# Optimization experiments

Measured on AMD Instinct MI355X. Metric: run time of the kernel, lower is better.

The kernel has to match this reference:

```python
import jax, jax.numpy as jnp
import numpy as np

ENZ_DIM, CPD_DIM, OUT_DIM = 1280, 256, 512
B, L_ENZ, L_CPD = 32, 512, 128
SCALE = OUT_DIM ** 0.5


def _linear_params(key, d_in, d_out):
    k1, k2 = jax.random.split(key)
    lim = 1.0 / np.sqrt(d_in)
    W = jax.random.uniform(k1, (d_in, d_out), jnp.float32, -lim, lim)
    b = jax.random.uniform(k2, (d_out,), jnp.float32, -lim, lim)
    return W, b


def setup_inputs() -> dict:
    key = jax.random.key(0)
    ks = jax.random.split(key, 16)
    inp = {
        "enz_node_feature": jax.random.normal(ks[0], (B, L_ENZ, ENZ_DIM), jnp.float32),
        "substrate_node_feature": jax.random.normal(ks[1], (B, L_CPD, CPD_DIM), jnp.float32),
        "product_node_feature": jax.random.normal(ks[2], (B, L_CPD, CPD_DIM), jnp.float32),
        "enz_node_feature_mask": jnp.ones((B, L_ENZ), dtype=bool),
        "substrate_node_feature_mask": jnp.ones((B, L_CPD), dtype=bool),
        "product_node_feature_mask": jnp.ones((B, L_CPD), dtype=bool),
        "interaction_weight": jax.random.normal(ks[3], (B, L_CPD, L_ENZ), jnp.float32),
    }
    # cross_attn_enzyme: query=enz (ENZ_DIM), key/value=cpd (CPD_DIM)
    inp["enz_Wq"], inp["enz_bq"] = _linear_params(ks[4], ENZ_DIM, OUT_DIM)
    inp["enz_Wk"], inp["enz_bk"] = _linear_params(ks[5], CPD_DIM, OUT_DIM)
    inp["enz_Wv"], inp["enz_bv"] = _linear_params(ks[6], CPD_DIM, OUT_DIM)
    # cross_attn_substrate: query=cpd, key/value=enz
    inp["sub_Wq"], inp["sub_bq"] = _linear_params(ks[7], CPD_DIM, OUT_DIM)
    inp["sub_Wk"], inp["sub_bk"] = _linear_params(ks[8], ENZ_DIM, OUT_DIM)
    inp["sub_Wv"], inp["sub_bv"] = _linear_params(ks[9], ENZ_DIM, OUT_DIM)
    # cross_attn_product: query=cpd, key/value=enz
    inp["prod_Wq"], inp["prod_bq"] = _linear_params(ks[10], CPD_DIM, OUT_DIM)
    inp["prod_Wk"], inp["prod_bk"] = _linear_params(ks[11], ENZ_DIM, OUT_DIM)
    inp["prod_Wv"], inp["prod_bv"] = _linear_params(ks[12], ENZ_DIM, OUT_DIM)
    return inp


def _cross_attn(q_in, k_in, v_in, q_mask, k_mask, Wq, bq, Wk, bk, Wv, bv, attn_bias=None):
    q = q_in @ Wq + bq          # [B, Lq, D]
    k = k_in @ Wk + bk          # [B, Lk, D]
    v = v_in @ Wv + bv          # [B, Lk, D]
    scores = jnp.einsum("bqd,bkd->bqk", q, k) / SCALE
    if attn_bias is not None:
        scores = scores + attn_bias
    mask = q_mask[:, :, None] & k_mask[:, None, :]   # [B, Lq, Lk]
    scores = jnp.where(mask, scores, -1e9)
    w = jax.nn.softmax(scores, axis=-1)
    return jnp.einsum("bqk,bkd->bqd", w, v)


def reference(enz_node_feature, substrate_node_feature, product_node_feature,
              enz_node_feature_mask, substrate_node_feature_mask, product_node_feature_mask,
              interaction_weight,
              enz_Wq, enz_bq, enz_Wk, enz_bk, enz_Wv, enz_bv,
              sub_Wq, sub_bq, sub_Wk, sub_bk, sub_Wv, sub_bv,
              prod_Wq, prod_bq, prod_Wk, prod_bk, prod_Wv, prod_bv):
    subs_pocket_weight = interaction_weight                       # [B, L_cpd, L_enz]
    pocket_subs_weight = jnp.swapaxes(interaction_weight, 1, 2)   # [B, L_enz, L_cpd]

    enzyme_subs = _cross_attn(enz_node_feature, substrate_node_feature, substrate_node_feature,
                              enz_node_feature_mask, substrate_node_feature_mask,
                              enz_Wq, enz_bq, enz_Wk, enz_bk, enz_Wv, enz_bv,
                              attn_bias=pocket_subs_weight)
    subs_enzyme = _cross_attn(substrate_node_feature, enz_node_feature, enz_node_feature,
                              substrate_node_feature_mask, enz_node_feature_mask,
                              sub_Wq, sub_bq, sub_Wk, sub_bk, sub_Wv, sub_bv,
                              attn_bias=subs_pocket_weight)
    # product path reuses cross_attn_enzyme weights for enz->prod (as in torch code)
    enzyme_prod = _cross_attn(enz_node_feature, product_node_feature, product_node_feature,
                              enz_node_feature_mask, product_node_feature_mask,
                              enz_Wq, enz_bq, enz_Wk, enz_bk, enz_Wv, enz_bv)
    prod_enzyme = _cross_attn(product_node_feature, enz_node_feature, enz_node_feature,
                              product_node_feature_mask, enz_node_feature_mask,
                              prod_Wq, prod_bq, prod_Wk, prod_bk, prod_Wv, prod_bv)

    return jnp.concatenate([enzyme_subs.mean(axis=1), subs_enzyme.mean(axis=1),
                            enzyme_prod.mean(axis=1), prod_enzyme.mean(axis=1)], axis=-1)
```

## Files before the change

kernel.cpp:

```cpp
#include <hip/hip_runtime.h>
#include <cstdint>
#include <cstddef>


#define SCALE_INV 0.044194173824159216f

typedef short bf16x8 __attribute__((ext_vector_type(8)));
typedef float f32x4  __attribute__((ext_vector_type(4)));

__device__ __forceinline__ ushort f2bf(float f) {
  union { float f; unsigned u; } c; c.f = f;
  unsigned u = c.u + 0x7fffu + ((c.u >> 16) & 1u);
  return (ushort)(u >> 16);
}
__device__ __forceinline__ float bf2f(ushort h) {
  return __uint_as_float(((unsigned)h) << 16);
}
__device__ __forceinline__ void gload16(const ushort* g, ushort* l) {
  __builtin_amdgcn_global_load_lds(
      (const __attribute__((address_space(1))) void*)g,
      (__attribute__((address_space(3))) void*)l, 16, 0, 0);
}

__device__ __forceinline__ void cvt8(const float* __restrict__ in,
                                     ushort* __restrict__ out, int blk, int n) {
  int i = (blk * 256 + (int)threadIdx.x) * 8;
  if (i >= n) return;
  float4 a = *(const float4*)(in + i);
  float4 b = *(const float4*)(in + i + 4);
  ushort o[8] = { f2bf(a.x), f2bf(a.y), f2bf(a.z), f2bf(a.w),
                  f2bf(b.x), f2bf(b.y), f2bf(b.z), f2bf(b.w) };
  *(uint4*)(out + i) = *(uint4*)o;
}

__global__ __launch_bounds__(256) void prep_fused(
    const float* __restrict__ enz, const float* __restrict__ sub,
    const float* __restrict__ prod,
    ushort* __restrict__ enz_b, ushort* __restrict__ sub_b, ushort* __restrict__ prod_b,
    const float* __restrict__ enz_Wq, const float* __restrict__ enz_Wk,
    const float* __restrict__ sub_Wq, const float* __restrict__ sub_Wk,
    const float* __restrict__ prod_Wq, const float* __restrict__ prod_Wk,
    ushort* __restrict__ eWq_b, ushort* __restrict__ eWk_b,
    ushort* __restrict__ sWq_b, ushort* __restrict__ sWk_b,
    ushort* __restrict__ pWq_b, ushort* __restrict__ pWk_b,
    const float* __restrict__ enz_bq, const float* __restrict__ sub_bq,
    const float* __restrict__ prod_bq,
    const float* __restrict__ enz_bv, const float* __restrict__ sub_bv,
    const float* __restrict__ prod_bv,
    ushort* __restrict__ W3t, float* __restrict__ u_e_s,
    float* __restrict__ zero_base, float* __restrict__ out)
{
  const int f = blockIdx.x, t = threadIdx.x;
  if (f < 10240) { cvt8(enz, enz_b, f, 20971520); return; }
  if (f < 10752) { cvt8(sub, sub_b, f - 10240, 1048576); return; }
  if (f < 11264) { cvt8(prod, prod_b, f - 10752, 1048576); return; }
  if (f < 12416) {
    const int l = f - 11264;
    if (l < 320)       cvt8(enz_Wq,  eWq_b, l,        655360);
    else if (l < 640)  cvt8(sub_Wk,  sWk_b, l - 320,  655360);
    else if (l < 960)  cvt8(prod_Wk, pWk_b, l - 640,  655360);
    else if (l < 1024) cvt8(enz_Wk,  eWk_b, l - 960,  131072);
    else if (l < 1088) cvt8(sub_Wq,  sWq_b, l - 1024, 131072);
    else               cvt8(prod_Wq, pWq_b, l - 1088, 131072);
    return;
  }
  if (f < 12592) {
    const int g = f - 12416;
    const float* W; const float* bv; int d0, kind;
    if (g < 80)       { W = sub_Wk;  bv = sub_bq;  d0 = g * 16;         kind = 0; }
    else if (g < 160) { W = prod_Wk; bv = prod_bq; d0 = (g - 80) * 16;  kind = 1; }
    else              { W = enz_Wk;  bv = enz_bq;  d0 = (g - 160) * 16; kind = 2; }
    const int r = t >> 4, i = t & 15, d = d0 + r;
    const float* row = W + (size_t)d * 512;
    float s = 0.f;
#pragma unroll
    for (int j = 0; j < 32; j++) s += row[i + j * 16] * bv[i + j * 16];
    s += __shfl_xor(s, 1); s += __shfl_xor(s, 2);
    s += __shfl_xor(s, 4); s += __shfl_xor(s, 8);
    if (i == 0) {
      if (kind < 2) W3t[(size_t)(768 + kind) * 1280 + d] = f2bf(s);
      else          u_e_s[d] = s * SCALE_INV;
    }
    return;
  }
  if (f < 13168) { zero_base[(f - 12592) * 256 + t] = 0.f; return; }
  if (f < 13483) {
    const int idx = (f - 13168) * 256 + t;
    ((unsigned*)(W3t + (size_t)770 * 1280))[idx] = 0u;
    return;
  }
  {
    const int idx = (f - 13483) * 256 + t;
    const int col = idx & 2047;
    const int q = col >> 9, n = col & 511;
    const float* bvp = (q == 1) ? sub_bv : (q == 3) ? prod_bv : enz_bv;
    out[idx] = bvp[n];
  }
}

__device__ __forceinline__ void mfma_tile(
    const ushort* __restrict__ A, int lda,
    const ushort* __restrict__ Bt, int ldb, int K,
    int bm, int bn, ushort* AsBase, ushort* BsBase, f32x4 (&acc)[4][4])
{
  const int t = threadIdx.x, wave = t >> 6, lane = t & 63;
  const int srow = wave * 16 + (lane >> 2);
  const int sseg = (lane & 3) * 8;
  const ushort* Ag0 = A + (size_t)(bm + srow) * lda + sseg;
  const ushort* Ag1 = Ag0 + (size_t)64 * lda;
  const ushort* Bg0 = Bt + (size_t)(bn + srow) * ldb + sseg;
  const ushort* Bg1 = Bg0 + (size_t)64 * ldb;
  ushort* AsP0 = AsBase + srow * 32 + sseg;
  ushort* AsP1 = AsP0 + 64 * 32;
  ushort* BsP0 = BsBase + srow * 32 + sseg;
  ushort* BsP1 = BsP0 + 64 * 32;
  const int wm = (wave >> 1) * 64, wn = (wave & 1) * 64;
  const int fl = lane & 15, fq = lane >> 4;
  const bf16x8* ArP = (const bf16x8*)(AsBase + (wm + fl) * 32 + fq * 8);
  const bf16x8* BrP = (const bf16x8*)(BsBase + (wn + fl) * 32 + fq * 8);
  for (int k0 = 0; k0 < K; k0 += 32) {
    __syncthreads();
    gload16(Ag0 + k0, AsP0);
    gload16(Ag1 + k0, AsP1);
    gload16(Bg0 + k0, BsP0);
    gload16(Bg1 + k0, BsP1);
    __syncthreads();
    bf16x8 af[4], bfr[4];
#pragma unroll
    for (int i = 0; i < 4; i++) af[i] = ArP[i * 64];
#pragma unroll
    for (int j = 0; j < 4; j++) bfr[j] = BrP[j * 64];
#pragma unroll
    for (int i = 0; i < 4; i++)
#pragma unroll
      for (int j = 0; j < 4; j++)
        acc[i][j] = __builtin_amdgcn_mfma_f32_16x16x32_bf16(af[i], bfr[j], acc[i][j], 0, 0, 0);
  }
}

__global__ __launch_bounds__(256) void fold_w3(
    const ushort* __restrict__ eWq_b, const ushort* __restrict__ eWk_b,
    const ushort* __restrict__ sWq_b, const ushort* __restrict__ sWk_b,
    const ushort* __restrict__ pWq_b, const ushort* __restrict__ pWk_b,
    ushort* __restrict__ W3t)
{
  __shared__ __align__(16) ushort As[128 * 32];
  __shared__ __align__(16) ushort Bs[128 * 32];
  const int f = blockIdx.x, seg = f / 20, l = f % 20;
  const int bm = (l / 10) * 128, bn = (l % 10) * 128;
  const ushort* A  = (seg == 0) ? eWk_b : (seg == 1) ? sWq_b : pWq_b;
  const ushort* Bt = (seg == 0) ? eWq_b : (seg == 1) ? sWk_b : pWk_b;
  f32x4 acc[4][4] = {};
  mfma_tile(A, 512, Bt, 512, 512, bm, bn, As, Bs, acc);
  const int lane = threadIdx.x & 63, wave = threadIdx.x >> 6;
  const int wm = (wave >> 1) * 64, wn = (wave & 1) * 64;
  const int fl = lane & 15, fq = lane >> 4;
#pragma unroll
  for (int i = 0; i < 4; i++)
#pragma unroll
    for (int j = 0; j < 4; j++) {
      const int col = bn + wn + j * 16 + fl;
#pragma unroll
      for (int r = 0; r < 4; r++) {
        const int row = seg * 256 + bm + wm + i * 16 + fq * 4 + r;
        W3t[(size_t)row * 1280 + col] = f2bf(acc[i][j][r]);
      }
    }
}

__global__ __launch_bounds__(256) void y_gemm(
    const ushort* __restrict__ enz_b, const ushort* __restrict__ W3t,
    ushort* __restrict__ Y)
{
  __shared__ __align__(16) ushort As[128 * 32];
  __shared__ __align__(16) ushort Bs[128 * 32];
  const int f = blockIdx.x;
  const int xcd = f & 7, slot = f >> 3;
  const int bm = (xcd * 16 + slot / 7) * 128, bn = (slot % 7) * 128;
  f32x4 acc[4][4] = {};
  mfma_tile(enz_b, 1280, W3t, 1280, 1280, bm, bn, As, Bs, acc);
  const int lane = threadIdx.x & 63, wave = threadIdx.x >> 6;
  const int wm = (wave >> 1) * 64, wn = (wave & 1) * 64;
  const int fl = lane & 15, fq = lane >> 4;
#pragma unroll
  for (int i = 0; i < 4; i++)
#pragma unroll
    for (int j = 0; j < 4; j++) {
      const int col = bn + wn + j * 16 + fl;
#pragma unroll
      for (int r = 0; r < 4; r++) {
        const int row = bm + wm + i * 16 + fq * 4 + r;
        Y[(size_t)row * 896 + col] = f2bf(acc[i][j][r]);
      }
    }
}

__global__ __launch_bounds__(256) void score_fused(
    const ushort* __restrict__ Y, const ushort* __restrict__ sub_b,
    const ushort* __restrict__ prod_b, const float* __restrict__ iw,
    const float* __restrict__ u_e_s,
    float* __restrict__ Sc_se, float* __restrict__ Sc_pe,
    float* __restrict__ l_se, float* __restrict__ l_pe,
    float* __restrict__ wsum_es, float* __restrict__ wsum_ep)
{
  __shared__ __align__(16) ushort As[128 * 32];
  __shared__ __align__(16) ushort Bs[128 * 32];
  __shared__ float red[2][128];
  __shared__ float red2[2][128];
  __shared__ float tsh[128];
  const int f = blockIdx.x, t = threadIdx.x;
  const int lane = t & 63, wave = t >> 6;
  const int wm = (wave >> 1) * 64, wn = (wave & 1) * 64;
  const int fl = lane & 15, fq = lane >> 4;
  f32x4 acc[4][4] = {};

  if (f < 256) {
    const int path = f >> 7, l = f & 127, b = l & 31, mt = l >> 5;
    const int bm = mt * 128;
    const ushort* X = (path ? prod_b : sub_b) + (size_t)b * 32768;
    {
      const int col = t >> 1, half = t & 1;
      const ushort* xr = X + col * 256 + half * 128;
      const float* uu = u_e_s + half * 128;
      float s = 0.f;
      for (int c = 0; c < 128; c++) s += bf2f(xr[c]) * uu[c];
      s += __shfl_xor(s, 1);
      if (!half) tsh[col] = s;
    }
    mfma_tile(Y + (size_t)b * 512 * 896, 896, X, 256, 256, bm, 0, As, Bs, acc);
    const size_t ib = (size_t)b * 65536;
    float rsum[4][4];
#pragma unroll
    for (int i = 0; i < 4; i++)
#pragma unroll
      for (int r = 0; r < 4; r++) rsum[i][r] = 0.f;
#pragma unroll
    for (int i = 0; i < 4; i++)
#pragma unroll
      for (int j = 0; j < 4; j++)
#pragma unroll
        for (int r = 0; r < 4; r++) {
          const int row = wm + i * 16 + fq * 4 + r;
          const int col = wn + j * 16 + fl;
          float s = acc[i][j][r] * SCALE_INV + tsh[col];
          if (path == 0) s += iw[ib + (size_t)col * 512 + (bm + row)];
          const float e = __expf(s);
          acc[i][j][r] = e;
          rsum[i][r] += e;
        }
#pragma unroll
    for (int m = 1; m <= 8; m <<= 1)
#pragma unroll
      for (int i = 0; i < 4; i++)
#pragma unroll
        for (int r = 0; r < 4; r++)
          rsum[i][r] += __shfl_xor(rsum[i][r], m);
    if (fl == 0)
#pragma unroll
      for (int i = 0; i < 4; i++)
#pragma unroll
        for (int r = 0; r < 4; r++)
          red[wave & 1][wm + i * 16 + fq * 4 + r] = rsum[i][r];
    __syncthreads();
    float csum[4] = { 0.f, 0.f, 0.f, 0.f };
#pragma unroll
    for (int i = 0; i < 4; i++)
#pragma unroll
      for (int r = 0; r < 4; r++) {
        const int row = wm + i * 16 + fq * 4 + r;
        const float invr = 1.f / (red[0][row] + red[1][row]);
#pragma unroll
        for (int j = 0; j < 4; j++) csum[j] += acc[i][j][r] * invr;
      }
#pragma unroll
    for (int m = 16; m <= 32; m <<= 1)
#pragma unroll
      for (int j = 0; j < 4; j++) csum[j] += __shfl_xor(csum[j], m);
    if (fq == 0)
#pragma unroll
      for (int j = 0; j < 4; j++) red2[wave >> 1][wn + j * 16 + fl] = csum[j];
    __syncthreads();
    float* ws = (path ? wsum_ep : wsum_es) + b * 128;
    if (t < 128) atomicAdd(&ws[t], red2[0][t] + red2[1][t]);
  } else {
    const int g = f - 256, path = g >> 7, l = g & 127, b = l & 31, nt = l >> 5;
    const int bn = nt * 128;
    const ushort* A  = (path ? prod_b : sub_b) + (size_t)b * 32768;
    const ushort* Bt = Y + (size_t)b * 512 * 896 + 256 + path * 256;
    mfma_tile(A, 256, Bt, 896, 256, 0, bn, As, Bs, acc);
    const size_t ib = (size_t)b * 65536;
    float* Sc = (path ? Sc_pe : Sc_se) + ib;
    float tv[4];
#pragma unroll
    for (int j = 0; j < 4; j++) {
      const int col = wn + j * 16 + fl;
      tv[j] = bf2f(Y[(size_t)(b * 512 + bn + col) * 896 + 768 + path]) * SCALE_INV;
    }
    float rsum[4][4];
#pragma unroll
    for (int i = 0; i < 4; i++)
#pragma unroll
      for (int r = 0; r < 4; r++) rsum[i][r] = 0.f;
#pragma unroll
    for (int i = 0; i < 4; i++)
#pragma unroll
      for (int j = 0; j < 4; j++)
#pragma unroll
        for (int r = 0; r < 4; r++) {
          const int row = wm + i * 16 + fq * 4 + r;
          const int col = wn + j * 16 + fl;
          float s = acc[i][j][r] * SCALE_INV + tv[j];
          if (path == 0) s += iw[ib + (size_t)row * 512 + (bn + col)];
          const float e = __expf(s);
          Sc[(size_t)row * 512 + bn + col] = e;
          rsum[i][r] += e;
        }
#pragma unroll
    for (int m = 1; m <= 8; m <<= 1)
#pragma unroll
      for (int i = 0; i < 4; i++)
#pragma unroll
        for (int r = 0; r < 4; r++)
          rsum[i][r] += __shfl_xor(rsum[i][r], m);
    if (fl == 0)
#pragma unroll
      for (int i = 0; i < 4; i++)
#pragma unroll
        for (int r = 0; r < 4; r++)
          red[wave & 1][wm + i * 16 + fq * 4 + r] = rsum[i][r];
    __syncthreads();
    float* lr = (path ? l_pe : l_se) + b * 128;
    if (t < 128) atomicAdd(&lr[t], red[0][t] + red[1][t]);
  }
}

__global__ __launch_bounds__(256) void colsum2(
    const float* __restrict__ Sc_se, const float* __restrict__ Sc_pe,
    const float* __restrict__ l_se, const float* __restrict__ l_pe,
    float* __restrict__ wsum_se, float* __restrict__ wsum_pe)
{
  __shared__ float inv[32];
  const int f = blockIdx.x, t = threadIdx.x;
  const int path = f >> 7, l = f & 127, b = l & 31, qc = l >> 5;
  const float* Sc = (path ? Sc_pe : Sc_se) + (size_t)b * 65536 + (size_t)(qc * 32) * 512;
  const float* lv = (path ? l_pe : l_se) + b * 128 + qc * 32;
  float* ws = (path ? wsum_pe : wsum_se) + b * 512;
  if (t < 32) inv[t] = 1.f / lv[t];
  __syncthreads();
  float a0 = 0.f, a1 = 0.f;
  for (int q = 0; q < 32; q++) {
    const float iq = inv[q];
    a0 += Sc[(size_t)q * 512 + t] * iq;
    a1 += Sc[(size_t)q * 512 + 256 + t] * iq;
  }
  atomicAdd(&ws[t], a0);
  atomicAdd(&ws[t + 256], a1);
}

__global__ __launch_bounds__(256) void wx_fused(
    const float* __restrict__ wsum_se, const float* __restrict__ wsum_pe,
    const float* __restrict__ wsum_es, const float* __restrict__ wsum_ep,
    const ushort* __restrict__ enz_b, const ushort* __restrict__ sub_b,
    const ushort* __restrict__ prod_b,
    float* __restrict__ wx_se, float* __restrict__ wx_pe,
    float* __restrict__ wx_es, float* __restrict__ wx_ep)
{
  __shared__ float wse[256], wpe[256];
  const int f = blockIdx.x, t = threadIdx.x;
  if (f < 320) {
    const int ch = f % 5, tmp = f / 5, b = tmp & 31, kh = tmp >> 5;
    wse[t] = wsum_se[b * 512 + kh * 256 + t];
    wpe[t] = wsum_pe[b * 512 + kh * 256 + t];
    __syncthreads();
    const int c = ch * 256 + t;
    const ushort* X = enz_b + (size_t)b * 512 * 1280 + (size_t)(kh * 256) * 1280 + c;
    float a_se = 0.f, a_pe = 0.f;
    for (int k = 0; k < 256; k++) {
      const float x = bf2f(X[(size_t)k * 1280]);
      a_se += wse[k] * x;
      a_pe += wpe[k] * x;
    }
    atomicAdd(&wx_se[b * 1280 + c], a_se);
    atomicAdd(&wx_pe[b * 1280 + c], a_pe);
  } else if (f < 352) {
    const int b = f - 320;
    const ushort* X = sub_b + (size_t)b * 128 * 256 + t;
    float a = 0.f;
    for (int k = 0; k < 128; k++) a += wsum_es[b * 128 + k] * bf2f(X[(size_t)k * 256]);
    wx_es[b * 256 + t] = a;
  } else {
    const int b = f - 352;
    const ushort* X = prod_b + (size_t)b * 128 * 256 + t;
    float a = 0.f;
    for (int k = 0; k < 128; k++) a += wsum_ep[b * 128 + k] * bf2f(X[(size_t)k * 256]);
    wx_ep[b * 256 + t] = a;
  }
}

__global__ __launch_bounds__(256) void out_gemv(
    const float* __restrict__ wx_es, const float* __restrict__ wx_se,
    const float* __restrict__ wx_ep, const float* __restrict__ wx_pe,
    const float* __restrict__ enz_Wv, const float* __restrict__ sub_Wv,
    const float* __restrict__ prod_Wv,
    float* __restrict__ out)
{
  __shared__ float sw[32][64];
  const int f = blockIdx.x, t = threadIdx.x;
  const float* wx; const float* Wv; int Cdim, qoff, nb, cc; float inv;
  if (f < 40)      { wx = wx_se; Wv = sub_Wv;  Cdim = 1280; inv = 1.f / 128.f; qoff = 512;  nb = f & 1;        cc = f >> 1; }
  else if (f < 80) { wx = wx_pe; Wv = prod_Wv; Cdim = 1280; inv = 1.f / 128.f; qoff = 1536; nb = (f - 40) & 1; cc = (f - 40) >> 1; }
  else if (f < 88) { wx = wx_es; Wv = enz_Wv;  Cdim = 256;  inv = 1.f / 512.f; qoff = 0;    nb = (f - 80) & 1; cc = (f - 80) >> 1; }
  else             { wx = wx_ep; Wv = enz_Wv;  Cdim = 256;  inv = 1.f / 512.f; qoff = 1024; nb = (f - 88) & 1; cc = (f - 88) >> 1; }
  const int c0 = cc * 64, n = nb * 256 + t;
#pragma unroll
  for (int i = 0; i < 8; i++) {
    const int idx = t + i * 256, b = idx >> 6, c = idx & 63;
    sw[b][c] = wx[(size_t)b * Cdim + c0 + c];
  }
  __syncthreads();
  float acc[32];
#pragma unroll
  for (int b = 0; b < 32; b++) acc[b] = 0.f;
  for (int c = 0; c < 64; c += 4) {
    const float w0 = Wv[(size_t)(c0 + c) * 512 + n];
    const float w1 = Wv[(size_t)(c0 + c + 1) * 512 + n];
    const float w2 = Wv[(size_t)(c0 + c + 2) * 512 + n];
    const float w3 = Wv[(size_t)(c0 + c + 3) * 512 + n];
#pragma unroll
    for (int b = 0; b < 32; b++) {
      const float4 s = *(const float4*)&sw[b][c];
      acc[b] += s.x * w0 + s.y * w1 + s.z * w2 + s.w * w3;
    }
  }
#pragma unroll
  for (int b = 0; b < 32; b++)
    atomicAdd(&out[(size_t)b * 2048 + qoff + n], acc[b] * inv);
}

extern "C" void kernel_launch(void* const* d_in, const int* in_sizes, int n_in,
                              void* d_out, int out_size, void* d_ws, size_t ws_size,
                              hipStream_t stream)
{
  (void)in_sizes; (void)n_in; (void)out_size; (void)ws_size;
  const float* enz     = (const float*)d_in[0];
  const float* sub     = (const float*)d_in[1];
  const float* prod    = (const float*)d_in[2];
  const float* iw      = (const float*)d_in[6];
  const float* enz_Wq  = (const float*)d_in[7];
  const float* enz_bq  = (const float*)d_in[8];
  const float* enz_Wk  = (const float*)d_in[9];
  const float* enz_Wv  = (const float*)d_in[11];
  const float* enz_bv  = (const float*)d_in[12];
  const float* sub_Wq  = (const float*)d_in[13];
  const float* sub_bq  = (const float*)d_in[14];
  const float* sub_Wk  = (const float*)d_in[15];
  const float* sub_Wv  = (const float*)d_in[17];
  const float* sub_bv  = (const float*)d_in[18];
  const float* prod_Wq = (const float*)d_in[19];
  const float* prod_bq = (const float*)d_in[20];
  const float* prod_Wk = (const float*)d_in[21];
  const float* prod_Wv = (const float*)d_in[23];
  const float* prod_bv = (const float*)d_in[24];
  float* out = (float*)d_out;

  char* wsb = (char*)d_ws;
  size_t off = 0;
  auto alloc = [&](size_t bytes) {
    void* p = wsb + off;
    off += (bytes + 255) & ~(size_t)255;
    return p;
  };
  ushort* enz_b   = (ushort*)alloc((size_t)32 * 512 * 1280 * 2);
  ushort* sub_b   = (ushort*)alloc((size_t)32 * 128 * 256 * 2);
  ushort* prod_b  = (ushort*)alloc((size_t)32 * 128 * 256 * 2);
  ushort* eWq_b   = (ushort*)alloc((size_t)1280 * 512 * 2);
  ushort* sWk_b   = (ushort*)alloc((size_t)1280 * 512 * 2);
  ushort* pWk_b   = (ushort*)alloc((size_t)1280 * 512 * 2);
  ushort* eWk_b   = (ushort*)alloc((size_t)256 * 512 * 2);
  ushort* sWq_b   = (ushort*)alloc((size_t)256 * 512 * 2);
  ushort* pWq_b   = (ushort*)alloc((size_t)256 * 512 * 2);
  ushort* W3t     = (ushort*)alloc((size_t)896 * 1280 * 2);
  ushort* Y       = (ushort*)alloc((size_t)16384 * 896 * 2);
  float*  u_e_s   = (float*)alloc(256 * 4);
  float*  Sc_se   = (float*)alloc((size_t)32 * 128 * 512 * 4);
  float*  Sc_pe   = (float*)alloc((size_t)32 * 128 * 512 * 4);
  float* wsum_es = (float*)alloc(4096 * 4);
  float* wsum_ep = (float*)alloc(4096 * 4);
  float* wsum_se = (float*)alloc(16384 * 4);
  float* wsum_pe = (float*)alloc(16384 * 4);
  float* l_se    = (float*)alloc(4096 * 4);
  float* l_pe    = (float*)alloc(4096 * 4);
  float* wx_se   = (float*)alloc(40960 * 4);
  float* wx_pe   = (float*)alloc(40960 * 4);
  float* wx_es   = (float*)alloc(8192 * 4);
  float* wx_ep   = (float*)alloc(8192 * 4);

  const dim3 blk(256);

  prep_fused<<<13739, blk, 0, stream>>>(
      enz, sub, prod, enz_b, sub_b, prod_b,
      enz_Wq, enz_Wk, sub_Wq, sub_Wk, prod_Wq, prod_Wk,
      eWq_b, eWk_b, sWq_b, sWk_b, pWq_b, pWk_b,
      enz_bq, sub_bq, prod_bq, enz_bv, sub_bv, prod_bv,
      W3t, u_e_s, wsum_es, out);

  fold_w3<<<60, blk, 0, stream>>>(eWq_b, eWk_b, sWq_b, sWk_b, pWq_b, pWk_b, W3t);

  y_gemm<<<896, blk, 0, stream>>>(enz_b, W3t, Y);

  score_fused<<<512, blk, 0, stream>>>(
      Y, sub_b, prod_b, iw, u_e_s, Sc_se, Sc_pe, l_se, l_pe, wsum_es, wsum_ep);

  colsum2<<<256, blk, 0, stream>>>(Sc_se, Sc_pe, l_se, l_pe, wsum_se, wsum_pe);

  wx_fused<<<384, blk, 0, stream>>>(
      wsum_se, wsum_pe, wsum_es, wsum_ep, enz_b, sub_b, prod_b,
      wx_se, wx_pe, wx_es, wx_ep);

  out_gemv<<<96, blk, 0, stream>>>(
      wx_es, wx_se, wx_ep, wx_pe, enz_Wv, sub_Wv, prod_Wv, out);
}
```

Baseline: 333.3 us.

## Rewrite y_gemm as 256x256 tile, 512-thread, double-buffered async-LDS GEMM

Replaces the 128x128 y_gemm built on the shared mfma_tile helper with a dedicated 256x256-tile kernel. It uses 8 waves, 128KB of dynamic LDS with double buffering, XOR-swizzled LDS layout, direct global-to-LDS loads and wave priority hints. The Y and W3t row pitch is padded from 896 to 1024 so N tiles divide evenly, and waves with nothing to do in the final partial tile skip their MFMAs. Downstream kernels and the zero-fill range are updated for the new pitch. This raises arithmetic intensity and overlaps loads with compute, at the cost of larger padded buffers, extra zeroing, and wasted tiles in the last N block.

```diff
diff --git a/kernel.cpp b/kernel.cpp
--- a/kernel.cpp
+++ b/kernel.cpp
@@ -84,13 +84,13 @@
     return;
   }
   if (f < 13168) { zero_base[(f - 12592) * 256 + t] = 0.f; return; }
-  if (f < 13483) {
+  if (f < 13803) {
     const int idx = (f - 13168) * 256 + t;
     ((unsigned*)(W3t + (size_t)770 * 1280))[idx] = 0u;
     return;
   }
   {
-    const int idx = (f - 13483) * 256 + t;
+    const int idx = (f - 13803) * 256 + t;
     const int col = idx & 2047;
     const int q = col >> 9, n = col & 511;
     const float* bvp = (q == 1) ? sub_bv : (q == 3) ? prod_bv : enz_bv;
@@ -168,29 +168,117 @@
     }
 }
 
-__global__ __launch_bounds__(256) void y_gemm(
-    const ushort* __restrict__ enz_b, const ushort* __restrict__ W3t,
+__device__ __forceinline__ void yg_stage_half(
+    const ushort* __restrict__ gbase, int k0, int h,
+    ushort* ldsTile, int wv, int l, int srow8, int scol)
+{
+  const int row0 = h * 128 + wv * 16 + srow8;
+  const ushort* g0 = gbase + (size_t)row0 * 1280 + k0 + scol;
+  ushort* d0 = ldsTile + h * 8192 + wv * 1024 + l * 8;
+  gload16(g0, d0);
+  gload16(g0 + (size_t)8 * 1280, d0 + 512);
+}
+
+__device__ __forceinline__ bf16x8 yg_frag(const ushort* tile, int row, int kk, int fq) {
+  const int X = (kk * 64 + fq * 16) ^ ((row & 7) << 4);
+  return *(const bf16x8*)((const char*)tile + row * 128 + X);
+}
+
+__global__ __launch_bounds__(512, 2) void y_gemm(
+    const ushort* __restrict__ A,
+    const ushort* __restrict__ B,
     ushort* __restrict__ Y)
 {
-  __shared__ __align__(16) ushort As[128 * 32];
-  __shared__ __align__(16) ushort Bs[128 * 32];
+  extern __shared__ __align__(16) ushort lds[];
+  const int t = threadIdx.x;
+  const int wv = t >> 6, l = t & 63;
+  const int fl = l & 15, fq = l >> 4;
   const int f = blockIdx.x;
   const int xcd = f & 7, slot = f >> 3;
-  const int bm = (xcd * 16 + slot / 7) * 128, bn = (slot % 7) * 128;
-  f32x4 acc[4][4] = {};
-  mfma_tile(enz_b, 1280, W3t, 1280, 1280, bm, bn, As, Bs, acc);
-  const int lane = threadIdx.x & 63, wave = threadIdx.x >> 6;
-  const int wm = (wave >> 1) * 64, wn = (wave & 1) * 64;
-  const int fl = lane & 15, fq = lane >> 4;
-#pragma unroll
-  for (int i = 0; i < 4; i++)
-#pragma unroll
-    for (int j = 0; j < 4; j++) {
-      const int col = bn + wn + j * 16 + fl;
-#pragma unroll
-      for (int r = 0; r < 4; r++) {
-        const int row = bm + wm + i * 16 + fq * 4 + r;
-        Y[(size_t)row * 896 + col] = f2bf(acc[i][j][r]);
+  const int mt = xcd * 8 + (slot >> 2), nt = slot & 3;
+  const int bm = mt * 256, bn = nt * 256;
+  const int wm = (wv >> 2) * 128, wn = (wv & 3) * 64;
+  const int nfr = (bn != 768) ? 4 : (((wv & 3) == 0) ? 1 : 0);
+  const int srow8 = l >> 3;
+  const int scol = 8 * ((l & 7) ^ srow8);
+  const ushort* Ag = A + (size_t)bm * 1280;
+  const ushort* Bg = B + (size_t)bn * 1280;
+
+  f32x4 acc[8][4] = {};
+
+  yg_stage_half(Ag, 0, 0, lds, wv, l, srow8, scol);
+  yg_stage_half(Ag, 0, 1, lds, wv, l, srow8, scol);
+  yg_stage_half(Bg, 0, 0, lds + 16384, wv, l, srow8, scol);
+  yg_stage_half(Bg, 0, 1, lds + 16384, wv, l, srow8, scol);
+  yg_stage_half(Ag, 64, 0, lds + 32768, wv, l, srow8, scol);
+  yg_stage_half(Ag, 64, 1, lds + 32768, wv, l, srow8, scol);
+  asm volatile("s_waitcnt vmcnt(4)" ::: "memory");
+  __builtin_amdgcn_s_barrier();
+  __builtin_amdgcn_sched_barrier(0);
+
+  for (int j = 0; j < 20; ++j) {
+    const int p = j & 1;
+    const ushort* At = lds + p * 32768;
+    const ushort* Bt = At + 16384;
+    ushort* Ao = (ushort*)(lds + (p ^ 1) * 32768);
+    ushort* Bo = Ao + 16384;
+    const int kn = (j + 1) * 64;
+
+    if (j < 19) yg_stage_half(Bg, kn, 0, Bo, wv, l, srow8, scol);
+    bf16x8 bf_[4][2];
+    if (nfr > 0) {
+#pragma unroll
+      for (int n = 0; n < 4; ++n) if (n < nfr)
+#pragma unroll
+        for (int kk = 0; kk < 2; ++kk)
+          bf_[n][kk] = yg_frag(Bt, wn + n * 16 + fl, kk, fq);
+    }
+#pragma unroll
+    for (int mp = 0; mp < 4; ++mp) {
+      if (mp == 1 && j < 19) yg_stage_half(Bg, kn, 1, Bo, wv, l, srow8, scol);
+      if (nfr > 0) {
+        bf16x8 a0[2], a1[2];
+#pragma unroll
+        for (int kk = 0; kk < 2; ++kk) {
+          a0[kk] = yg_frag(At, wm + (mp * 2) * 16 + fl, kk, fq);
+          a1[kk] = yg_frag(At, wm + (mp * 2 + 1) * 16 + fl, kk, fq);
+        }
+        __builtin_amdgcn_s_setprio(1);
+#pragma unroll
+        for (int n = 0; n < 4; ++n) if (n < nfr) {
+#pragma unroll
+          for (int kk = 0; kk < 2; ++kk) {
+            acc[mp * 2][n] = __builtin_amdgcn_mfma_f32_16x16x32_bf16(
+                a0[kk], bf_[n][kk], acc[mp * 2][n], 0, 0, 0);
+            acc[mp * 2 + 1][n] = __builtin_amdgcn_mfma_f32_16x16x32_bf16(
+                a1[kk], bf_[n][kk], acc[mp * 2 + 1][n], 0, 0, 0);
+          }
+        }
+        __builtin_amdgcn_s_setprio(0);
+      }
+    }
+
+    asm volatile("" ::: "memory");
+    __builtin_amdgcn_s_barrier();
+    if (j + 2 < 20) {
+      yg_stage_half(Ag, (j + 2) * 64, 0, (ushort*)At, wv, l, srow8, scol);
+      yg_stage_half(Ag, (j + 2) * 64, 1, (ushort*)At, wv, l, srow8, scol);
+    }
+    if (j < 18) asm volatile("s_waitcnt vmcnt(4)" ::: "memory");
+    else        asm volatile("s_waitcnt vmcnt(0)" ::: "memory");
+    __builtin_amdgcn_s_barrier();
+    __builtin_amdgcn_sched_barrier(0);
+  }
+
+#pragma unroll
+  for (int m = 0; m < 8; ++m)
+#pragma unroll
+    for (int n = 0; n < 4; ++n) if (n < nfr) {
+#pragma unroll
+      for (int r = 0; r < 4; ++r) {
+        const int row = bm + wm + m * 16 + fq * 4 + r;
+        const int col = bn + wn + n * 16 + fl;
+        Y[(size_t)row * 1024 + col] = f2bf(acc[m][n][r]);
       }
     }
 }
@@ -227,7 +315,7 @@
       s += __shfl_xor(s, 1);
       if (!half) tsh[col] = s;
     }
-    mfma_tile(Y + (size_t)b * 512 * 896, 896, X, 256, 256, bm, 0, As, Bs, acc);
+    mfma_tile(Y + (size_t)b * 512 * 1024, 1024, X, 256, 256, bm, 0, As, Bs, acc);
     const size_t ib = (size_t)b * 65536;
     float rsum[4][4];
 #pragma unroll
@@ -286,15 +374,15 @@
     const int g = f - 256, path = g >> 7, l = g & 127, b = l & 31, nt = l >> 5;
     const int bn = nt * 128;
     const ushort* A  = (path ? prod_b : sub_b) + (size_t)b * 32768;
-    const ushort* Bt = Y + (size_t)b * 512 * 896 + 256 + path * 256;
-    mfma_tile(A, 256, Bt, 896, 256, 0, bn, As, Bs, acc);
+    const ushort* Bt = Y + (size_t)b * 512 * 1024 + 256 + path * 256;
+    mfma_tile(A, 256, Bt, 1024, 256, 0, bn, As, Bs, acc);
     const size_t ib = (size_t)b * 65536;
     float* Sc = (path ? Sc_pe : Sc_se) + ib;
     float tv[4];
 #pragma unroll
     for (int j = 0; j < 4; j++) {
       const int col = wn + j * 16 + fl;
-      tv[j] = bf2f(Y[(size_t)(b * 512 + bn + col) * 896 + 768 + path]) * SCALE_INV;
+      tv[j] = bf2f(Y[(size_t)(b * 512 + bn + col) * 1024 + 768 + path]) * SCALE_INV;
     }
     float rsum[4][4];
 #pragma unroll
@@ -479,8 +567,8 @@
   ushort* eWk_b   = (ushort*)alloc((size_t)256 * 512 * 2);
   ushort* sWq_b   = (ushort*)alloc((size_t)256 * 512 * 2);
   ushort* pWq_b   = (ushort*)alloc((size_t)256 * 512 * 2);
-  ushort* W3t     = (ushort*)alloc((size_t)896 * 1280 * 2);
-  ushort* Y       = (ushort*)alloc((size_t)16384 * 896 * 2);
+  ushort* W3t     = (ushort*)alloc((size_t)1024 * 1280 * 2);
+  ushort* Y       = (ushort*)alloc((size_t)16384 * 1024 * 2);
   float*  u_e_s   = (float*)alloc(256 * 4);
   float*  Sc_se   = (float*)alloc((size_t)32 * 128 * 512 * 4);
   float*  Sc_pe   = (float*)alloc((size_t)32 * 128 * 512 * 4);
@@ -495,9 +583,16 @@
   float* wx_es   = (float*)alloc(8192 * 4);
   float* wx_ep   = (float*)alloc(8192 * 4);
 
+  static bool ygemm_attr_set = false;
+  if (!ygemm_attr_set) {
+    hipFuncSetAttribute(reinterpret_cast<const void*>(y_gemm),
+                        hipFuncAttributeMaxDynamicSharedMemorySize, 131072);
+    ygemm_attr_set = true;
+  }
+
   const dim3 blk(256);
 
-  prep_fused<<<13739, blk, 0, stream>>>(
+  prep_fused<<<14059, blk, 0, stream>>>(
       enz, sub, prod, enz_b, sub_b, prod_b,
       enz_Wq, enz_Wk, sub_Wq, sub_Wk, prod_Wq, prod_Wk,
       eWq_b, eWk_b, sWq_b, sWk_b, pWq_b, pWk_b,
@@ -506,7 +601,7 @@
 
   fold_w3<<<60, blk, 0, stream>>>(eWq_b, eWk_b, sWq_b, sWk_b, pWq_b, pWk_b, W3t);
 
-  y_gemm<<<896, blk, 0, stream>>>(enz_b, W3t, Y);
+  y_gemm<<<256, 512, 131072, stream>>>(enz_b, W3t, Y);
 
   score_fused<<<512, blk, 0, stream>>>(
       Y, sub_b, prod_b, iw, u_e_s, Sc_se, Sc_pe, l_se, l_pe, wsum_es, wsum_ep);
```

Result: faster. 313.1 us (-6.1%).
